# Kernel tuning notes

Measured on AMD Instinct MI355X. Metric: run time of the kernel, lower is better.

Reference implementation:

```python
import jax, jax.numpy as jnp
import numpy as np

B, C_IN, H, W = 8, 64, 256, 256
C_OUT, K, N_KERNELS = 128, 3, 8
PAD = K // 2


def setup_inputs() -> dict:
    key = jax.random.key(0)
    k1, k2, k3, k4 = jax.random.split(key, 4)
    x = jax.random.normal(k1, (B, C_IN, H, W), dtype=jnp.float32)
    kernel_bank = jax.random.normal(k2, (N_KERNELS, C_OUT, C_IN, K, K), dtype=jnp.float32)
    # nn.Linear(in_channels, num_kernels): weight (N, C_IN), bias (N,)
    lim = 1.0 / np.sqrt(C_IN)
    attn_w = jax.random.uniform(k3, (N_KERNELS, C_IN), minval=-lim, maxval=lim, dtype=jnp.float32)
    attn_b = jax.random.uniform(k4, (N_KERNELS,), minval=-lim, maxval=lim, dtype=jnp.float32)
    return {"x": x, "kernel_bank": kernel_bank, "attn_w": attn_w, "attn_b": attn_b}


def _per_sample_conv(xi, wi):
    # xi: (C_IN, H, W), wi: (C_OUT, C_IN, K, K)
    out = jax.lax.conv_general_dilated(
        xi[None], wi, window_strides=(1, 1), padding=[(PAD, PAD), (PAD, PAD)],
        dimension_numbers=("NCHW", "OIHW", "NCHW"))
    return out[0]


def reference(x, kernel_bank, attn_w, attn_b):
    pooled = jnp.mean(x, axis=(2, 3))                      # (B, C_IN)
    logits = pooled @ attn_w.T + attn_b                     # (B, N)
    attn = jax.nn.softmax(logits, axis=1)                   # (B, N)
    # Fused kernel mix: avoid (B, N, O, I, K, K) intermediate
    mixed = jnp.einsum("bn,noihw->boihw", attn, kernel_bank)  # (B, O, I, K, K)
    return jax.vmap(_per_sample_conv)(x, mixed)             # (B, O, H, W)
```

## Files before the change

kernel.cpp:

```cpp
#include <hip/hip_runtime.h>
#include <hip/hip_bf16.h>

#define B_     8
#define C_IN   64
#define C_OUT  128
#define HW     256
#define NK     8
#define KS     3

typedef __attribute__((ext_vector_type(8))) short bf16x8;
typedef __attribute__((ext_vector_type(4))) float f32x4;
typedef __attribute__((ext_vector_type(4))) unsigned int u32x4;

__device__ inline unsigned short f2bf(float f) {
    union { float f; unsigned int u; } a; a.f = f;
    unsigned int u = a.u;
    u += 0x7fffu + ((u >> 16) & 1u);
    return (unsigned short)(u >> 16);
}
__device__ inline float bf2f(unsigned short u) {
    union { float f; unsigned int u; } a; a.u = ((unsigned int)u) << 16; return a.f;
}

#define XT_PLANE  (258 * 64)
#define SLAB_B    16640

__global__ __launch_bounds__(256) void prepass_kernel(const float* __restrict__ x,
                                                      unsigned short* __restrict__ xT,
                                                      float* __restrict__ poolpart) {
    const int hp = blockIdx.x;
    const int b  = blockIdx.y;
    const int t  = threadIdx.x;
    unsigned short* plane = xT + ((size_t)b * 258 + hp) * XT_PLANE;

    if (hp == 0 || hp == 257) {
        f32x4 z = {0.f, 0.f, 0.f, 0.f};
        for (int ofs = t * 16; ofs < XT_PLANE * 2; ofs += 256 * 16)
            *(f32x4*)((char*)plane + ofs) = z;
        return;
    }
    const int h = hp - 1;

    __shared__ unsigned short tile[256 * 66];
    __shared__ float psum[4][64];

    const float* xp = x + ((size_t)b * C_IN * HW + h) * HW + t;
    unsigned int pk[32];
    #pragma unroll
    for (int ci = 0; ci < 32; ci++) {
        float v0 = xp[(size_t)(2 * ci) * (HW * HW)];
        float v1 = xp[(size_t)(2 * ci + 1) * (HW * HW)];
        unsigned int p = (unsigned int)f2bf(v0) | ((unsigned int)f2bf(v1) << 16);
        pk[ci] = p;
        *(unsigned int*)&tile[t * 66 + 2 * ci] = p;
    }

    unsigned short* rowp = plane + (size_t)(t + 1) * 64;
    const int sw = (t + 1) & 7;
    #pragma unroll
    for (int j = 0; j < 8; j++) {
        u32x4 v; v[0] = pk[4*j]; v[1] = pk[4*j+1]; v[2] = pk[4*j+2]; v[3] = pk[4*j+3];
        *(u32x4*)(rowp + (size_t)((j ^ sw) * 8)) = v;
    }
    if (t < 2) {
        unsigned short* zr = plane + (size_t)(t ? 257 : 0) * 64;
        f32x4 z = {0.f, 0.f, 0.f, 0.f};
        #pragma unroll
        for (int j = 0; j < 8; j++) *(f32x4*)((char*)zr + j * 16) = z;
    }

    __syncthreads();
    const int c = t & 63, part = t >> 6;
    float s = 0.f;
    #pragma unroll 8
    for (int i = 0; i < 64; i++)
        s += bf2f(tile[(part * 64 + i) * 66 + c]);
    psum[part][c] = s;
    __syncthreads();
    if (t < 64)
        poolpart[((size_t)b * 258 + hp) * 64 + t] =
            (psum[0][t] + psum[1][t]) + (psum[2][t] + psum[3][t]);
}

__global__ __launch_bounds__(256) void attn_kernel(const float* __restrict__ poolpart,
                                                   const float* __restrict__ attn_w,
                                                   const float* __restrict__ attn_b,
                                                   float* __restrict__ attn) {
    const int b = blockIdx.x;
    const int t = threadIdx.x;
    const int c = t & 63, part = t >> 6;
    __shared__ float psum[4][64];
    __shared__ float pooled[64];
    __shared__ float logits[NK];

    float s = 0.f;
    const float* pp = poolpart + ((size_t)b * 258) * 64 + c;
    for (int hp = part * 64 + 1; hp <= part * 64 + 64; hp++)
        s += pp[(size_t)hp * 64];
    psum[part][c] = s;
    __syncthreads();
    if (t < 64)
        pooled[t] = ((psum[0][t] + psum[1][t]) + (psum[2][t] + psum[3][t]))
                    * (1.0f / (HW * HW));
    __syncthreads();
    if (t < NK) {
        float l = attn_b[t];
        #pragma unroll 8
        for (int cc = 0; cc < C_IN; cc++) l += pooled[cc] * attn_w[t * C_IN + cc];
        logits[t] = l;
    }
    __syncthreads();
    if (t < NK) {
        float m = -1e30f;
        #pragma unroll
        for (int j = 0; j < NK; j++) m = fmaxf(m, logits[j]);
        float denom = 0.f;
        #pragma unroll
        for (int j = 0; j < NK; j++) denom += expf(logits[j] - m);
        attn[b * NK + t] = expf(logits[t] - m) / denom;
    }
}

__global__ __launch_bounds__(256) void mix_kernel(const float* __restrict__ bank,
                                                  const float* __restrict__ attn,
                                                  unsigned short* __restrict__ Wt2) {
    const int PER_B = C_OUT * C_IN * KS * KS;
    int idx = blockIdx.x * 256 + threadIdx.x;
    int b = idx / PER_B;
    int r = idx % PER_B;
    float s = 0.f;
    #pragma unroll
    for (int n = 0; n < NK; n++) s += attn[b * NK + n] * bank[(size_t)n * PER_B + r];
    int kw = r % 3;
    int t1 = r / 3;
    int kh = t1 % 3;
    int t2 = t1 / 3;
    int i = t2 & 63;
    int o = t2 >> 6;
    size_t off = (((size_t)((b * 3 + kh) * 3 + kw) * 2 + (i >> 5)) * 128 + o) * 32 + (i & 31);
    Wt2[off] = f2bf(s);
}

__global__ __launch_bounds__(512, 4) void conv_mfma3(const unsigned short* __restrict__ xT,
                                                     const short* __restrict__ Wt2,
                                                     float* __restrict__ out) {
    const int w0 = blockIdx.x * 128;
    const int h0 = blockIdx.y * 8;
    const int b  = blockIdx.z;
    const int t    = threadIdx.x;
    const int lane = t & 63;
    const int wid  = t >> 6;
    const int wm   = (wid >> 1) * 32;
    const int wn   = (wid & 1) * 64;
    const int l15  = lane & 15;
    const int quad = lane >> 4;

    __shared__ short sxs[4 * 8320];

    #define STAGE(HP) do {                                                            \
        const char* _src = (const char*)(xT + (((size_t)b * 258 + (size_t)(HP)) * 258 \
                                               + (size_t)w0) * 64);                   \
        char* _dst = (char*)sxs + (((HP) & 3) * SLAB_B);                              \
        const int _wo = wid * 2048;                                                   \
        __builtin_amdgcn_global_load_lds((const __attribute__((address_space(1))) void*)(_src + _wo +        lane * 16), (__attribute__((address_space(3))) void*)(_dst + _wo),        16, 0, 0); \
        __builtin_amdgcn_global_load_lds((const __attribute__((address_space(1))) void*)(_src + _wo + 1024 + lane * 16), (__attribute__((address_space(3))) void*)(_dst + _wo + 1024), 16, 0, 0); \
        if (wid == 7)                                                                 \
            __builtin_amdgcn_global_load_lds((const __attribute__((address_space(1))) void*)(_src + 16384 + lane * 4),   (__attribute__((address_space(3))) void*)(_dst + 16384),        4, 0, 0); \
    } while (0)

    const short* wt_b = Wt2 + (size_t)b * (9 * 2 * 4096);

    STAGE(h0); STAGE(h0 + 1); STAGE(h0 + 2);

    #pragma unroll 1
    for (int h = h0; h < h0 + 8; ++h) {
        __builtin_amdgcn_s_barrier();
        if (h <= h0 + 6) {
            STAGE(h + 3);
            if (wid == 7) asm volatile("s_waitcnt vmcnt(3)" ::: "memory");
            else          asm volatile("s_waitcnt vmcnt(2)" ::: "memory");
        } else {
            asm volatile("s_waitcnt vmcnt(0)" ::: "memory");
        }
        __builtin_amdgcn_s_barrier();

        f32x4 acc[2][4];
        #pragma unroll
        for (int mt = 0; mt < 2; mt++)
            #pragma unroll
            for (int nt = 0; nt < 4; nt++)
                acc[mt][nt] = (f32x4){0.f, 0.f, 0.f, 0.f};

        #pragma unroll
        for (int kh = 0; kh < 3; kh++) {
            const short* buf = sxs + ((h + kh) & 3) * 8320;
            const short* wbase = wt_b + kh * (3 * 2 * 4096);
            #pragma unroll
            for (int kw = 0; kw < 3; kw++) {
                const int row = wn + l15 + kw;
                const int rx  = row & 7;
                #pragma unroll
                for (int ic = 0; ic < 2; ic++) {
                    const short* Ap = wbase + (kw * 2 + ic) * 4096 + (wm + l15) * 32 + quad * 8;
                    bf16x8 a0 = *(const bf16x8*)(Ap);
                    bf16x8 a1 = *(const bf16x8*)(Ap + 512);
                    const short* Bp = buf + row * 64 + (((ic << 2) + quad) ^ rx) * 8;
                    bf16x8 b0 = *(const bf16x8*)(Bp);
                    bf16x8 b1 = *(const bf16x8*)(Bp + 1024);
                    bf16x8 b2 = *(const bf16x8*)(Bp + 2048);
                    bf16x8 b3 = *(const bf16x8*)(Bp + 3072);
                    acc[0][0] = __builtin_amdgcn_mfma_f32_16x16x32_bf16(a0, b0, acc[0][0], 0, 0, 0);
                    acc[0][1] = __builtin_amdgcn_mfma_f32_16x16x32_bf16(a0, b1, acc[0][1], 0, 0, 0);
                    acc[0][2] = __builtin_amdgcn_mfma_f32_16x16x32_bf16(a0, b2, acc[0][2], 0, 0, 0);
                    acc[0][3] = __builtin_amdgcn_mfma_f32_16x16x32_bf16(a0, b3, acc[0][3], 0, 0, 0);
                    acc[1][0] = __builtin_amdgcn_mfma_f32_16x16x32_bf16(a1, b0, acc[1][0], 0, 0, 0);
                    acc[1][1] = __builtin_amdgcn_mfma_f32_16x16x32_bf16(a1, b1, acc[1][1], 0, 0, 0);
                    acc[1][2] = __builtin_amdgcn_mfma_f32_16x16x32_bf16(a1, b2, acc[1][2], 0, 0, 0);
                    acc[1][3] = __builtin_amdgcn_mfma_f32_16x16x32_bf16(a1, b3, acc[1][3], 0, 0, 0);
                }
            }
        }

        #pragma unroll
        for (int mt = 0; mt < 2; mt++) {
            const int o = wm + mt * 16 + quad * 4;
            #pragma unroll
            for (int nt = 0; nt < 4; nt++) {
                const int w = w0 + wn + nt * 16 + l15;
                float* op = out + (((size_t)(b * C_OUT + o) * HW + h) * HW + w);
                #pragma unroll
                for (int r = 0; r < 4; r++) op[(size_t)r * HW * HW] = acc[mt][nt][r];
            }
        }
    }
    #undef STAGE
}

__global__ __launch_bounds__(256) void pool_kernel(const float* __restrict__ x,
                                                   float* __restrict__ pooled) {
    const int plane = blockIdx.x;
    const float4* p = (const float4*)(x + (size_t)plane * HW * HW);
    float s = 0.f;
    for (int idx = threadIdx.x; idx < (HW * HW) / 4; idx += 256) {
        float4 v = p[idx];
        s += v.x + v.y + v.z + v.w;
    }
    #pragma unroll
    for (int off = 32; off > 0; off >>= 1) s += __shfl_down(s, off, 64);
    __shared__ float ls[4];
    const int lane = threadIdx.x & 63, wv = threadIdx.x >> 6;
    if (lane == 0) ls[wv] = s;
    __syncthreads();
    if (threadIdx.x == 0) {
        float t = ls[0] + ls[1] + ls[2] + ls[3];
        pooled[plane] = t * (1.0f / (HW * HW));
    }
}

__global__ void attn_legacy(const float* __restrict__ pooled,
                            const float* __restrict__ attn_w,
                            const float* __restrict__ attn_b,
                            float* __restrict__ attn) {
    const int t = threadIdx.x;
    const int b = t >> 3, n = t & 7;
    float s = attn_b[n];
    #pragma unroll 8
    for (int c = 0; c < C_IN; c++) s += pooled[b * C_IN + c] * attn_w[n * C_IN + c];
    __shared__ float logits[B_ * NK];
    logits[t] = s;
    __syncthreads();
    float m = -1e30f;
    #pragma unroll
    for (int j = 0; j < NK; j++) m = fmaxf(m, logits[b * NK + j]);
    float denom = 0.f;
    #pragma unroll
    for (int j = 0; j < NK; j++) denom += expf(logits[b * NK + j] - m);
    attn[t] = expf(s - m) / denom;
}

__global__ __launch_bounds__(256) void conv_mfma(const float* __restrict__ x,
                                                 const short* __restrict__ Wt2,
                                                 float* __restrict__ out) {
    const int w0 = blockIdx.x * 128;
    const int h  = blockIdx.y;
    const int b  = blockIdx.z;
    const int t    = threadIdx.x;
    const int lane = t & 63;
    const int wid  = t >> 6;
    const int wm   = (wid & 1) * 64;
    const int wn   = (wid >> 1) * 64;
    const int l15  = lane & 15;
    const int quad = lane >> 4;
    __shared__ short sxs[130 * 72];
    f32x4 acc[4][4];
    #pragma unroll
    for (int mt = 0; mt < 4; mt++)
        #pragma unroll
        for (int nt = 0; nt < 4; nt++)
            acc[mt][nt] = (f32x4){0.f, 0.f, 0.f, 0.f};
    for (int kh = 0; kh < 3; kh++) {
        __syncthreads();
        const int hr = h + kh - 1;
        const bool rv = (hr >= 0) && (hr < HW);
        {
            const int wl = t & 127;
            const int w  = w0 + wl - 1;
            const bool wvalid = rv && (w >= 0) && (w < HW);
            #pragma unroll
            for (int it = 0; it < 16; it++) {
                const int ip = it * 2 + (t >> 7);
                float v0 = 0.f, v1 = 0.f;
                if (wvalid) {
                    const float* px = x + (((size_t)(b * C_IN + 2 * ip) * HW + hr) * HW + w);
                    v0 = px[0];
                    v1 = px[HW * HW];
                }
                ushort2 u;
                u.x = f2bf(v0);
                u.y = f2bf(v1);
                *(ushort2*)&sxs[wl * 72 + 2 * ip] = u;
            }
            if (t < 128) {
                const int i2  = t >> 1;
                const int wl2 = 128 + (t & 1);
                const int w2  = w0 + wl2 - 1;
                unsigned short uv = 0;
                if (rv && w2 < HW)
                    uv = f2bf(x[((size_t)(b * C_IN + i2) * HW + hr) * HW + w2]);
                ((unsigned short*)sxs)[wl2 * 72 + i2] = uv;
            }
        }
        __syncthreads();
        const short* wbase = Wt2 + (size_t)((b * 3 + kh) * 3) * 2 * 4096;
        #pragma unroll
        for (int kw = 0; kw < 3; kw++) {
            #pragma unroll
            for (int ic = 0; ic < 2; ic++) {
                const short* Ap = wbase + (size_t)(kw * 2 + ic) * 4096
                                + (wm + l15) * 32 + quad * 8;
                bf16x8 a0 = *(const bf16x8*)(Ap);
                bf16x8 a1 = *(const bf16x8*)(Ap + 512);
                bf16x8 a2 = *(const bf16x8*)(Ap + 1024);
                bf16x8 a3 = *(const bf16x8*)(Ap + 1536);
                const short* Bp = sxs + (wn + l15 + kw) * 72 + ic * 32 + quad * 8;
                bf16x8 b0 = *(const bf16x8*)(Bp);
                bf16x8 b1 = *(const bf16x8*)(Bp + 16 * 72);
                bf16x8 b2 = *(const bf16x8*)(Bp + 32 * 72);
                bf16x8 b3 = *(const bf16x8*)(Bp + 48 * 72);
                acc[0][0] = __builtin_amdgcn_mfma_f32_16x16x32_bf16(a0, b0, acc[0][0], 0, 0, 0);
                acc[0][1] = __builtin_amdgcn_mfma_f32_16x16x32_bf16(a0, b1, acc[0][1], 0, 0, 0);
                acc[0][2] = __builtin_amdgcn_mfma_f32_16x16x32_bf16(a0, b2, acc[0][2], 0, 0, 0);
                acc[0][3] = __builtin_amdgcn_mfma_f32_16x16x32_bf16(a0, b3, acc[0][3], 0, 0, 0);
                acc[1][0] = __builtin_amdgcn_mfma_f32_16x16x32_bf16(a1, b0, acc[1][0], 0, 0, 0);
                acc[1][1] = __builtin_amdgcn_mfma_f32_16x16x32_bf16(a1, b1, acc[1][1], 0, 0, 0);
                acc[1][2] = __builtin_amdgcn_mfma_f32_16x16x32_bf16(a1, b2, acc[1][2], 0, 0, 0);
                acc[1][3] = __builtin_amdgcn_mfma_f32_16x16x32_bf16(a1, b3, acc[1][3], 0, 0, 0);
                acc[2][0] = __builtin_amdgcn_mfma_f32_16x16x32_bf16(a2, b0, acc[2][0], 0, 0, 0);
                acc[2][1] = __builtin_amdgcn_mfma_f32_16x16x32_bf16(a2, b1, acc[2][1], 0, 0, 0);
                acc[2][2] = __builtin_amdgcn_mfma_f32_16x16x32_bf16(a2, b2, acc[2][2], 0, 0, 0);
                acc[2][3] = __builtin_amdgcn_mfma_f32_16x16x32_bf16(a2, b3, acc[2][3], 0, 0, 0);
                acc[3][0] = __builtin_amdgcn_mfma_f32_16x16x32_bf16(a3, b0, acc[3][0], 0, 0, 0);
                acc[3][1] = __builtin_amdgcn_mfma_f32_16x16x32_bf16(a3, b1, acc[3][1], 0, 0, 0);
                acc[3][2] = __builtin_amdgcn_mfma_f32_16x16x32_bf16(a3, b2, acc[3][2], 0, 0, 0);
                acc[3][3] = __builtin_amdgcn_mfma_f32_16x16x32_bf16(a3, b3, acc[3][3], 0, 0, 0);
            }
        }
    }
    #pragma unroll
    for (int mt = 0; mt < 4; mt++) {
        const int o = wm + mt * 16 + quad * 4;
        #pragma unroll
        for (int nt = 0; nt < 4; nt++) {
            const int w = w0 + wn + nt * 16 + l15;
            float* op = out + (((size_t)(b * C_OUT + o) * HW + h) * HW + w);
            #pragma unroll
            for (int r = 0; r < 4; r++) op[(size_t)r * HW * HW] = acc[mt][nt][r];
        }
    }
}

extern "C" void kernel_launch(void* const* d_in, const int* in_sizes, int n_in,
                              void* d_out, int out_size, void* d_ws, size_t ws_size,
                              hipStream_t stream) {
    const float* x      = (const float*)d_in[0];
    const float* bank   = (const float*)d_in[1];
    const float* attn_w = (const float*)d_in[2];
    const float* attn_b = (const float*)d_in[3];
    float* out = (float*)d_out;

    const size_t XT_BYTES  = (size_t)B_ * 258 * XT_PLANE * sizeof(short);
    const size_t WT2_BYTES = (size_t)B_ * C_OUT * C_IN * KS * KS * sizeof(short);
    const size_t PP_BYTES  = (size_t)B_ * 258 * 64 * sizeof(float);
    const size_t NEED = XT_BYTES + WT2_BYTES + PP_BYTES + (size_t)(B_ * NK) * 4 + 256;

    if (ws_size >= NEED) {
        unsigned short* xT  = (unsigned short*)d_ws;
        unsigned short* Wt2 = (unsigned short*)((char*)d_ws + XT_BYTES);
        float* poolpart = (float*)((char*)d_ws + XT_BYTES + WT2_BYTES);
        float* attn     = poolpart + (size_t)B_ * 258 * 64;

        prepass_kernel<<<dim3(258, B_), 256, 0, stream>>>(x, xT, poolpart);
        attn_kernel<<<B_, 256, 0, stream>>>(poolpart, attn_w, attn_b, attn);
        mix_kernel<<<(B_ * C_OUT * C_IN * KS * KS) / 256, 256, 0, stream>>>(bank, attn, Wt2);
        conv_mfma3<<<dim3(2, HW / 8, B_), 512, 0, stream>>>(xT, (const short*)Wt2, out);
    } else {
        unsigned short* Wt2 = (unsigned short*)d_ws;
        float* pooled = (float*)((char*)d_ws + 589824 * sizeof(short));
        float* attn   = pooled + B_ * C_IN;
        pool_kernel<<<B_ * C_IN, 256, 0, stream>>>(x, pooled);
        attn_legacy<<<1, 64, 0, stream>>>(pooled, attn_w, attn_b, attn);
        mix_kernel<<<(B_ * C_OUT * C_IN * KS * KS) / 256, 256, 0, stream>>>(bank, attn, Wt2);
        conv_mfma<<<dim3(2, HW, B_), 256, 0, stream>>>(x, (const short*)Wt2, out);
    }
}
```

Before: 495.1 us.

## Use 4-wave blocks with 64x64 warp tiles and register-pipelined weight fragments

```diff
diff --git a/kernel.cpp b/kernel.cpp
--- a/kernel.cpp
+++ b/kernel.cpp
@@ -141,7 +141,7 @@
     Wt2[off] = f2bf(s);
 }
 
-__global__ __launch_bounds__(512, 4) void conv_mfma3(const unsigned short* __restrict__ xT,
+__global__ __launch_bounds__(256, 2) void conv_mfma4(const unsigned short* __restrict__ xT,
                                                      const short* __restrict__ Wt2,
                                                      float* __restrict__ out) {
     const int w0 = blockIdx.x * 128;
@@ -150,8 +150,8 @@
     const int t    = threadIdx.x;
     const int lane = t & 63;
     const int wid  = t >> 6;
-    const int wm   = (wid >> 1) * 32;
-    const int wn   = (wid & 1) * 64;
+    const int wm   = (wid & 1) * 64;
+    const int wn   = (wid >> 1) * 64;
     const int l15  = lane & 15;
     const int quad = lane >> 4;
 
@@ -161,68 +161,87 @@
         const char* _src = (const char*)(xT + (((size_t)b * 258 + (size_t)(HP)) * 258 \
                                                + (size_t)w0) * 64);                   \
         char* _dst = (char*)sxs + (((HP) & 3) * SLAB_B);                              \
-        const int _wo = wid * 2048;                                                   \
+        const int _wo = wid * 4096;                                                   \
         __builtin_amdgcn_global_load_lds((const __attribute__((address_space(1))) void*)(_src + _wo +        lane * 16), (__attribute__((address_space(3))) void*)(_dst + _wo),        16, 0, 0); \
         __builtin_amdgcn_global_load_lds((const __attribute__((address_space(1))) void*)(_src + _wo + 1024 + lane * 16), (__attribute__((address_space(3))) void*)(_dst + _wo + 1024), 16, 0, 0); \
-        if (wid == 7)                                                                 \
-            __builtin_amdgcn_global_load_lds((const __attribute__((address_space(1))) void*)(_src + 16384 + lane * 4),   (__attribute__((address_space(3))) void*)(_dst + 16384),        4, 0, 0); \
+        __builtin_amdgcn_global_load_lds((const __attribute__((address_space(1))) void*)(_src + _wo + 2048 + lane * 16), (__attribute__((address_space(3))) void*)(_dst + _wo + 2048), 16, 0, 0); \
+        __builtin_amdgcn_global_load_lds((const __attribute__((address_space(1))) void*)(_src + _wo + 3072 + lane * 16), (__attribute__((address_space(3))) void*)(_dst + _wo + 3072), 16, 0, 0); \
+        __builtin_amdgcn_global_load_lds((const __attribute__((address_space(1))) void*)(_src + 16384 + lane * 4),       (__attribute__((address_space(3))) void*)(_dst + 16384),        4, 0, 0); \
     } while (0)
 
-    const short* wt_b = Wt2 + (size_t)b * (9 * 2 * 4096);
+    const short* wt_b  = Wt2 + (size_t)b * (9 * 2 * 4096);
+    const short* Abase = wt_b + (wm + l15) * 32 + quad * 8;
+
+    bf16x8 Ab[3][4];
+    #pragma unroll
+    for (int q = 0; q < 2; q++)
+        #pragma unroll
+        for (int m = 0; m < 4; m++)
+            Ab[q][m] = *(const bf16x8*)(Abase + q * 4096 + m * 512);
 
     STAGE(h0); STAGE(h0 + 1); STAGE(h0 + 2);
 
     #pragma unroll 1
     for (int h = h0; h < h0 + 8; ++h) {
         __builtin_amdgcn_s_barrier();
-        if (h <= h0 + 6) {
+        if (h == h0) {
             STAGE(h + 3);
-            if (wid == 7) asm volatile("s_waitcnt vmcnt(3)" ::: "memory");
-            else          asm volatile("s_waitcnt vmcnt(2)" ::: "memory");
+            asm volatile("s_waitcnt vmcnt(5)" ::: "memory");
+        } else if (h <= h0 + 6) {
+            STAGE(h + 3);
+            asm volatile("s_waitcnt vmcnt(63)" ::: "memory");
         } else {
             asm volatile("s_waitcnt vmcnt(0)" ::: "memory");
         }
         __builtin_amdgcn_s_barrier();
 
-        f32x4 acc[2][4];
-        #pragma unroll
-        for (int mt = 0; mt < 2; mt++)
+        f32x4 acc[4][4];
+        #pragma unroll
+        for (int mt = 0; mt < 4; mt++)
             #pragma unroll
             for (int nt = 0; nt < 4; nt++)
                 acc[mt][nt] = (f32x4){0.f, 0.f, 0.f, 0.f};
 
         #pragma unroll
-        for (int kh = 0; kh < 3; kh++) {
+        for (int s = 0; s < 18; s++) {
+            const int kh = s / 6;
+            const int kw = (s % 6) >> 1;
+            const int ic = s & 1;
+            const int cbuf = s % 3;
+            const int nbuf = (s + 2) % 3;
+            const int ns   = (s + 2) % 18;
+            #pragma unroll
+            for (int m = 0; m < 4; m++)
+                Ab[nbuf][m] = *(const bf16x8*)(Abase + ns * 4096 + m * 512);
+
             const short* buf = sxs + ((h + kh) & 3) * 8320;
-            const short* wbase = wt_b + kh * (3 * 2 * 4096);
-            #pragma unroll
-            for (int kw = 0; kw < 3; kw++) {
-                const int row = wn + l15 + kw;
-                const int rx  = row & 7;
-                #pragma unroll
-                for (int ic = 0; ic < 2; ic++) {
-                    const short* Ap = wbase + (kw * 2 + ic) * 4096 + (wm + l15) * 32 + quad * 8;
-                    bf16x8 a0 = *(const bf16x8*)(Ap);
-                    bf16x8 a1 = *(const bf16x8*)(Ap + 512);
-                    const short* Bp = buf + row * 64 + (((ic << 2) + quad) ^ rx) * 8;
-                    bf16x8 b0 = *(const bf16x8*)(Bp);
-                    bf16x8 b1 = *(const bf16x8*)(Bp + 1024);
-                    bf16x8 b2 = *(const bf16x8*)(Bp + 2048);
-                    bf16x8 b3 = *(const bf16x8*)(Bp + 3072);
-                    acc[0][0] = __builtin_amdgcn_mfma_f32_16x16x32_bf16(a0, b0, acc[0][0], 0, 0, 0);
-                    acc[0][1] = __builtin_amdgcn_mfma_f32_16x16x32_bf16(a0, b1, acc[0][1], 0, 0, 0);
-                    acc[0][2] = __builtin_amdgcn_mfma_f32_16x16x32_bf16(a0, b2, acc[0][2], 0, 0, 0);
-                    acc[0][3] = __builtin_amdgcn_mfma_f32_16x16x32_bf16(a0, b3, acc[0][3], 0, 0, 0);
-                    acc[1][0] = __builtin_amdgcn_mfma_f32_16x16x32_bf16(a1, b0, acc[1][0], 0, 0, 0);
-                    acc[1][1] = __builtin_amdgcn_mfma_f32_16x16x32_bf16(a1, b1, acc[1][1], 0, 0, 0);
-                    acc[1][2] = __builtin_amdgcn_mfma_f32_16x16x32_bf16(a1, b2, acc[1][2], 0, 0, 0);
-                    acc[1][3] = __builtin_amdgcn_mfma_f32_16x16x32_bf16(a1, b3, acc[1][3], 0, 0, 0);
-                }
-            }
-        }
-
-        #pragma unroll
-        for (int mt = 0; mt < 2; mt++) {
+            const int row = wn + l15 + kw;
+            const short* Bp = buf + row * 64 + ((((ic << 2) + quad) ^ (row & 7))) * 8;
+            bf16x8 b0 = *(const bf16x8*)(Bp);
+            bf16x8 b1 = *(const bf16x8*)(Bp + 1024);
+            bf16x8 b2 = *(const bf16x8*)(Bp + 2048);
+            bf16x8 b3 = *(const bf16x8*)(Bp + 3072);
+
+            acc[0][0] = __builtin_amdgcn_mfma_f32_16x16x32_bf16(Ab[cbuf][0], b0, acc[0][0], 0, 0, 0);
+            acc[0][1] = __builtin_amdgcn_mfma_f32_16x16x32_bf16(Ab[cbuf][0], b1, acc[0][1], 0, 0, 0);
+            acc[0][2] = __builtin_amdgcn_mfma_f32_16x16x32_bf16(Ab[cbuf][0], b2, acc[0][2], 0, 0, 0);
+            acc[0][3] = __builtin_amdgcn_mfma_f32_16x16x32_bf16(Ab[cbuf][0], b3, acc[0][3], 0, 0, 0);
+            acc[1][0] = __builtin_amdgcn_mfma_f32_16x16x32_bf16(Ab[cbuf][1], b0, acc[1][0], 0, 0, 0);
+            acc[1][1] = __builtin_amdgcn_mfma_f32_16x16x32_bf16(Ab[cbuf][1], b1, acc[1][1], 0, 0, 0);
+            acc[1][2] = __builtin_amdgcn_mfma_f32_16x16x32_bf16(Ab[cbuf][1], b2, acc[1][2], 0, 0, 0);
+            acc[1][3] = __builtin_amdgcn_mfma_f32_16x16x32_bf16(Ab[cbuf][1], b3, acc[1][3], 0, 0, 0);
+            acc[2][0] = __builtin_amdgcn_mfma_f32_16x16x32_bf16(Ab[cbuf][2], b0, acc[2][0], 0, 0, 0);
+            acc[2][1] = __builtin_amdgcn_mfma_f32_16x16x32_bf16(Ab[cbuf][2], b1, acc[2][1], 0, 0, 0);
+            acc[2][2] = __builtin_amdgcn_mfma_f32_16x16x32_bf16(Ab[cbuf][2], b2, acc[2][2], 0, 0, 0);
+            acc[2][3] = __builtin_amdgcn_mfma_f32_16x16x32_bf16(Ab[cbuf][2], b3, acc[2][3], 0, 0, 0);
+            acc[3][0] = __builtin_amdgcn_mfma_f32_16x16x32_bf16(Ab[cbuf][3], b0, acc[3][0], 0, 0, 0);
+            acc[3][1] = __builtin_amdgcn_mfma_f32_16x16x32_bf16(Ab[cbuf][3], b1, acc[3][1], 0, 0, 0);
+            acc[3][2] = __builtin_amdgcn_mfma_f32_16x16x32_bf16(Ab[cbuf][3], b2, acc[3][2], 0, 0, 0);
+            acc[3][3] = __builtin_amdgcn_mfma_f32_16x16x32_bf16(Ab[cbuf][3], b3, acc[3][3], 0, 0, 0);
+        }
+
+        #pragma unroll
+        for (int mt = 0; mt < 4; mt++) {
             const int o = wm + mt * 16 + quad * 4;
             #pragma unroll
             for (int nt = 0; nt < 4; nt++) {
@@ -402,7 +421,7 @@
         prepass_kernel<<<dim3(258, B_), 256, 0, stream>>>(x, xT, poolpart);
         attn_kernel<<<B_, 256, 0, stream>>>(poolpart, attn_w, attn_b, attn);
         mix_kernel<<<(B_ * C_OUT * C_IN * KS * KS) / 256, 256, 0, stream>>>(bank, attn, Wt2);
-        conv_mfma3<<<dim3(2, HW / 8, B_), 512, 0, stream>>>(xT, (const short*)Wt2, out);
+        conv_mfma4<<<dim3(2, HW / 8, B_), 256, 0, stream>>>(xT, (const short*)Wt2, out);
     } else {
         unsigned short* Wt2 = (unsigned short*)d_ws;
         float* pooled = (float*)((char*)d_ws + 589824 * sizeof(short));
```

Measured after the change: 536.8 us. 1.08x slower.

## Replace LDS-pipelined conv with register-blocked direct-global MFMA kernel per output row

Applied to the files above, without the earlier changes.

```diff
diff --git a/kernel.cpp b/kernel.cpp
--- a/kernel.cpp
+++ b/kernel.cpp
@@ -23,7 +23,6 @@
 }
 
 #define XT_PLANE  (258 * 64)
-#define SLAB_B    16640
 
 __global__ __launch_bounds__(256) void prepass_kernel(const float* __restrict__ x,
                                                       unsigned short* __restrict__ xT,
@@ -141,99 +140,74 @@
     Wt2[off] = f2bf(s);
 }
 
-__global__ __launch_bounds__(512, 4) void conv_mfma3(const unsigned short* __restrict__ xT,
+__global__ __launch_bounds__(256, 2) void conv_mfma5(const unsigned short* __restrict__ xT,
                                                      const short* __restrict__ Wt2,
                                                      float* __restrict__ out) {
-    const int w0 = blockIdx.x * 128;
-    const int h0 = blockIdx.y * 8;
-    const int b  = blockIdx.z;
+    const int flat = blockIdx.y * HW + blockIdx.x;
+    const int work = (flat & 7) * (HW * B_ / 8) + (flat >> 3);
+    const int b = work >> 8;
+    const int h = work & 255;
+
     const int t    = threadIdx.x;
     const int lane = t & 63;
     const int wid  = t >> 6;
-    const int wm   = (wid >> 1) * 32;
-    const int wn   = (wid & 1) * 64;
     const int l15  = lane & 15;
     const int quad = lane >> 4;
-
-    __shared__ short sxs[4 * 8320];
-
-    #define STAGE(HP) do {                                                            \
-        const char* _src = (const char*)(xT + (((size_t)b * 258 + (size_t)(HP)) * 258 \
-                                               + (size_t)w0) * 64);                   \
-        char* _dst = (char*)sxs + (((HP) & 3) * SLAB_B);                              \
-        const int _wo = wid * 2048;                                                   \
-        __builtin_amdgcn_global_load_lds((const __attribute__((address_space(1))) void*)(_src + _wo +        lane * 16), (__attribute__((address_space(3))) void*)(_dst + _wo),        16, 0, 0); \
-        __builtin_amdgcn_global_load_lds((const __attribute__((address_space(1))) void*)(_src + _wo + 1024 + lane * 16), (__attribute__((address_space(3))) void*)(_dst + _wo + 1024), 16, 0, 0); \
-        if (wid == 7)                                                                 \
-            __builtin_amdgcn_global_load_lds((const __attribute__((address_space(1))) void*)(_src + 16384 + lane * 4),   (__attribute__((address_space(3))) void*)(_dst + 16384),        4, 0, 0); \
-    } while (0)
-
-    const short* wt_b = Wt2 + (size_t)b * (9 * 2 * 4096);
-
-    STAGE(h0); STAGE(h0 + 1); STAGE(h0 + 2);
-
-    #pragma unroll 1
-    for (int h = h0; h < h0 + 8; ++h) {
-        __builtin_amdgcn_s_barrier();
-        if (h <= h0 + 6) {
-            STAGE(h + 3);
-            if (wid == 7) asm volatile("s_waitcnt vmcnt(3)" ::: "memory");
-            else          asm volatile("s_waitcnt vmcnt(2)" ::: "memory");
-        } else {
-            asm volatile("s_waitcnt vmcnt(0)" ::: "memory");
-        }
-        __builtin_amdgcn_s_barrier();
-
-        f32x4 acc[2][4];
-        #pragma unroll
-        for (int mt = 0; mt < 2; mt++)
-            #pragma unroll
-            for (int nt = 0; nt < 4; nt++)
-                acc[mt][nt] = (f32x4){0.f, 0.f, 0.f, 0.f};
-
-        #pragma unroll
-        for (int kh = 0; kh < 3; kh++) {
-            const short* buf = sxs + ((h + kh) & 3) * 8320;
-            const short* wbase = wt_b + kh * (3 * 2 * 4096);
-            #pragma unroll
-            for (int kw = 0; kw < 3; kw++) {
-                const int row = wn + l15 + kw;
-                const int rx  = row & 7;
+    const int wn   = wid * 64;
+    const int r0   = wn + l15;
+
+    const short* Ab = Wt2 + (size_t)b * (9 * 2 * 4096) + l15 * 32 + quad * 8;
+    const unsigned short* xb = xT + (size_t)b * 258 * XT_PLANE;
+
+    f32x4 acc[8][4];
+    #pragma unroll
+    for (int m = 0; m < 8; m++)
+        #pragma unroll
+        for (int nt = 0; nt < 4; nt++)
+            acc[m][nt] = (f32x4){0.f, 0.f, 0.f, 0.f};
+
+    #pragma unroll
+    for (int kh = 0; kh < 3; kh++) {
+        const unsigned short* hpb = xb + (size_t)(h + kh) * XT_PLANE;
+        #pragma unroll
+        for (int kw = 0; kw < 3; kw++) {
+            const int rr = r0 + kw;
+            const unsigned short* rowb = hpb + rr * 64;
+            const int rx = rr & 7;
+            #pragma unroll
+            for (int ic = 0; ic < 2; ic++) {
+                const int s = (kh * 3 + kw) * 2 + ic;
+                bf16x8 Bv[4];
                 #pragma unroll
-                for (int ic = 0; ic < 2; ic++) {
-                    const short* Ap = wbase + (kw * 2 + ic) * 4096 + (wm + l15) * 32 + quad * 8;
-                    bf16x8 a0 = *(const bf16x8*)(Ap);
-                    bf16x8 a1 = *(const bf16x8*)(Ap + 512);
-                    const short* Bp = buf + row * 64 + (((ic << 2) + quad) ^ rx) * 8;
-                    bf16x8 b0 = *(const bf16x8*)(Bp);
-                    bf16x8 b1 = *(const bf16x8*)(Bp + 1024);
-                    bf16x8 b2 = *(const bf16x8*)(Bp + 2048);
-                    bf16x8 b3 = *(const bf16x8*)(Bp + 3072);
-                    acc[0][0] = __builtin_amdgcn_mfma_f32_16x16x32_bf16(a0, b0, acc[0][0], 0, 0, 0);
-                    acc[0][1] = __builtin_amdgcn_mfma_f32_16x16x32_bf16(a0, b1, acc[0][1], 0, 0, 0);
-                    acc[0][2] = __builtin_amdgcn_mfma_f32_16x16x32_bf16(a0, b2, acc[0][2], 0, 0, 0);
-                    acc[0][3] = __builtin_amdgcn_mfma_f32_16x16x32_bf16(a0, b3, acc[0][3], 0, 0, 0);
-                    acc[1][0] = __builtin_amdgcn_mfma_f32_16x16x32_bf16(a1, b0, acc[1][0], 0, 0, 0);
-                    acc[1][1] = __builtin_amdgcn_mfma_f32_16x16x32_bf16(a1, b1, acc[1][1], 0, 0, 0);
-                    acc[1][2] = __builtin_amdgcn_mfma_f32_16x16x32_bf16(a1, b2, acc[1][2], 0, 0, 0);
-                    acc[1][3] = __builtin_amdgcn_mfma_f32_16x16x32_bf16(a1, b3, acc[1][3], 0, 0, 0);
+                for (int nt = 0; nt < 4; nt++)
+                    Bv[nt] = *(const bf16x8*)(rowb + nt * 1024
+                                              + ((((ic << 2) + quad) ^ rx) << 3));
+                bf16x8 Av[8];
+                #pragma unroll
+                for (int m = 0; m < 8; m++)
+                    Av[m] = *(const bf16x8*)(Ab + s * 4096 + m * 512);
+                #pragma unroll
+                for (int m = 0; m < 8; m++) {
+                    #pragma unroll
+                    for (int nt = 0; nt < 4; nt++)
+                        acc[m][nt] = __builtin_amdgcn_mfma_f32_16x16x32_bf16(
+                            Av[m], Bv[nt], acc[m][nt], 0, 0, 0);
                 }
             }
         }
-
-        #pragma unroll
-        for (int mt = 0; mt < 2; mt++) {
-            const int o = wm + mt * 16 + quad * 4;
-            #pragma unroll
-            for (int nt = 0; nt < 4; nt++) {
-                const int w = w0 + wn + nt * 16 + l15;
-                float* op = out + (((size_t)(b * C_OUT + o) * HW + h) * HW + w);
-                #pragma unroll
-                for (int r = 0; r < 4; r++) op[(size_t)r * HW * HW] = acc[mt][nt][r];
-            }
-        }
-    }
-    #undef STAGE
+    }
+
+    #pragma unroll
+    for (int m = 0; m < 8; m++) {
+        const int o = m * 16 + quad * 4;
+        #pragma unroll
+        for (int nt = 0; nt < 4; nt++) {
+            const int w = wn + nt * 16 + l15;
+            float* op = out + (((size_t)(b * C_OUT + o) * HW + h) * HW + w);
+            #pragma unroll
+            for (int r = 0; r < 4; r++) op[(size_t)r * HW * HW] = acc[m][nt][r];
+        }
+    }
 }
 
 __global__ __launch_bounds__(256) void pool_kernel(const float* __restrict__ x,
@@ -402,7 +376,7 @@
         prepass_kernel<<<dim3(258, B_), 256, 0, stream>>>(x, xT, poolpart);
         attn_kernel<<<B_, 256, 0, stream>>>(poolpart, attn_w, attn_b, attn);
         mix_kernel<<<(B_ * C_OUT * C_IN * KS * KS) / 256, 256, 0, stream>>>(bank, attn, Wt2);
-        conv_mfma3<<<dim3(2, HW / 8, B_), 512, 0, stream>>>(xT, (const short*)Wt2, out);
+        conv_mfma5<<<dim3(HW, B_), 256, 0, stream>>>(xT, (const short*)Wt2, out);
     } else {
         unsigned short* Wt2 = (unsigned short*)d_ws;
         float* pooled = (float*)((char*)d_ws + 589824 * sizeof(short));
```

New measurement: 495.5 us. About the same (+0.1%).
